# Kernel tuning notes

Hardware: AMD Instinct MI355X
Metric: run time of the kernel (lower is better)

The kernel has to match this reference:

```python
import jax, jax.numpy as jnp
import numpy as np

B, S, E, H, C = 16, 2048, 128, 768, 457


def setup_inputs() -> dict:
    key = jax.random.key(0)
    ks = jax.random.split(key, 8)
    hidden_states = jax.random.normal(ks[0], (B, S, H), dtype=jnp.float32)
    field_labels = jax.random.randint(ks[1], (B, S), 0, C, dtype=jnp.int64) if jax.config.jax_enable_x64 else jax.random.randint(ks[1], (B, S), 0, C, dtype=jnp.int32)
    label_masks = jax.random.randint(ks[2], (B, S), 0, 2, dtype=jnp.int32)
    entities_attr = jax.random.randint(ks[3], (B, E), 0, C, dtype=jnp.int32)
    entities_list = (jax.random.uniform(ks[4], (B, S, E)) < 0.05).astype(jnp.int32)
    entities_len = jnp.maximum(entities_list.sum(axis=1), 1).astype(jnp.int32)  # (B, E)
    entities_mask = jax.random.randint(ks[5], (B, E), 0, 2).astype(bool)
    W = jax.random.normal(ks[6], (C, H), dtype=jnp.float32) * 0.02
    b = jax.random.normal(ks[7], (C,), dtype=jnp.float32) * 0.02
    return {"hidden_states": hidden_states, "field_labels": field_labels,
            "label_masks": label_masks, "entities_attr": entities_attr,
            "entities_list": entities_list, "entities_len": entities_len,
            "entities_mask": entities_mask, "W": W, "b": b}


def reference(hidden_states, field_labels, label_masks, entities_attr,
              entities_list, entities_len, entities_mask, W, b):
    # Entity mean-pool: torch does (B,E,S,H) expand*mul->sum; algebraically a bmm.
    dt = hidden_states.dtype
    ent_hidden = jnp.einsum('bsh,bse->beh', hidden_states, entities_list.astype(dt))
    ent_hidden = ent_hidden / entities_len.astype(dt)[..., None]        # (B,E,H)
    mc_logits = jnp.einsum('beh,ch->bec', ent_hidden, W) + b             # (B,E,C)
    # masked CrossEntropyLoss (mean over selected entities)
    logp = jax.nn.log_softmax(mc_logits, axis=-1)
    nll = -jnp.take_along_axis(logp, entities_attr[..., None].astype(jnp.int32), axis=-1)[..., 0]
    m = entities_mask.astype(dt)
    mask_loss = (nll * m).sum() / m.sum()
    return mask_loss
```

## Files before the change

### kernel.cpp

```cpp
#include <hip/hip_runtime.h>
#include <hip/hip_bf16.h>
#include <cstdint>
#include <cstddef>

constexpr int Bn = 16, Sn = 2048, En = 128, Hn = 768, Cn = 457;
constexpr int NP = 512;
using f32x4  = __attribute__((ext_vector_type(4))) float;
using bf16x8 = __attribute__((ext_vector_type(8))) short;

static __device__ inline unsigned short f2bf(float x) {
  __hip_bfloat16 b = __float2bfloat16(x);
  return *reinterpret_cast<unsigned short*>(&b);
}
static __device__ inline float bflo(unsigned int u) {
  unsigned int v = u << 16;
  return *reinterpret_cast<float*>(&v);
}
static __device__ inline float bfhi(unsigned int u) {
  unsigned int v = u & 0xFFFF0000u;
  return *reinterpret_cast<float*>(&v);
}

#define LGKM_BAR()                                            \
  do {                                                        \
    asm volatile("s_waitcnt lgkmcnt(0)" ::: "memory");        \
    __builtin_amdgcn_sched_barrier(0);                        \
    __builtin_amdgcn_s_barrier();                             \
    __builtin_amdgcn_sched_barrier(0);                        \
  } while (0)

__global__ __launch_bounds__(256) void pack_k(
    const int* __restrict__ el, unsigned int* __restrict__ pk2)
{
  const int l = threadIdx.x & 63;
  const int gw = blockIdx.x * 4 + (threadIdx.x >> 6);
  #pragma unroll 8
  for (int j = 0; j < 8; ++j) {
    const int tok = gw * 8 + j;
    const int b = tok >> 11, s = tok & 2047;
    const int v0 = el[(size_t)tok * 128 + l];
    const int v1 = el[(size_t)tok * 128 + 64 + l];
    const unsigned long long b0 = __ballot(v0 != 0);
    const unsigned long long b1 = __ballot(v1 != 0);
    if (l == 0) {
      unsigned int* p = pk2 + (size_t)b * 4 * Sn + s;
      p[0]          = (unsigned int)b0;
      p[Sn]         = (unsigned int)(b0 >> 32);
      p[2 * Sn]     = (unsigned int)b1;
      p[3 * Sn]     = (unsigned int)(b1 >> 32);
    }
  }
}

constexpr int PBN = 32, PBK2 = 64, PLD2 = 72;
constexpr int SCH = 4, SLEN = Sn / SCH, PNK2 = SLEN / PBK2;
__global__ __launch_bounds__(256, 6) void pool_k(
    const float* __restrict__ hidden,
    const unsigned int* __restrict__ pk2,
    unsigned short* __restrict__ entp)
{
  const int b = blockIdx.x, n0 = blockIdx.y * PBN, sc = blockIdx.z;
  const int s0 = sc * SLEN;
  const int tid = threadIdx.x, l = tid & 63, wv = tid >> 6;
  const int wm = wv >> 1, wn = wv & 1;

  __shared__ unsigned short Bs[2][PBN][PLD2];
  __shared__ unsigned int   PK2[4 * SLEN];

  {
    const int w = tid >> 6, off = (tid & 63) * 8;
    const unsigned int* srcp =
        pk2 + (size_t)b * 4 * Sn + (size_t)w * Sn + s0 + off;
    *reinterpret_cast<uint4*>(&PK2[w * SLEN + off]) =
        *reinterpret_cast<const uint4*>(srcp);
    *reinterpret_cast<uint4*>(&PK2[w * SLEN + off + 4]) =
        *reinterpret_cast<const uint4*>(srcp + 4);
  }

  const float* hb = hidden + ((size_t)b * Sn + s0) * Hn + n0;
  const int g = wv * 2 + (l >> 5), col = l & 31;

  auto loadh = [&](int kk, float (&f)[8]) {
    const int sb = kk * PBK2 + g * 8;
    #pragma unroll
    for (int i = 0; i < 8; ++i)
      f[i] = hb[(size_t)(sb + i) * Hn + col];
  };

  auto stage_b = [&](int bsel, const float (&f)[8]) {
    uint2 d0, d1;
    d0.x = (unsigned int)f2bf(f[0]) | ((unsigned int)f2bf(f[1]) << 16);
    d0.y = (unsigned int)f2bf(f[2]) | ((unsigned int)f2bf(f[3]) << 16);
    d1.x = (unsigned int)f2bf(f[4]) | ((unsigned int)f2bf(f[5]) << 16);
    d1.y = (unsigned int)f2bf(f[6]) | ((unsigned int)f2bf(f[7]) << 16);
    *reinterpret_cast<uint2*>(&Bs[bsel][col][g * 8])     = d0;
    *reinterpret_cast<uint2*>(&Bs[bsel][col][g * 8 + 4]) = d1;
  };

  f32x4 acc[4] = {};
  const int rl = l & 15, q = l >> 4, kr = q * 8;

  auto mfma_step = [&](int k, int cur) {
    #pragma unroll
    for (int ks = 0; ks < 2; ++ks) {
      const int sbase = k * PBK2 + ks * 32 + kr;
      const bf16x8 bfr = *reinterpret_cast<const bf16x8*>(
          &Bs[cur][wn * 16 + rl][ks * 32 + kr]);
      #pragma unroll
      for (int mp = 0; mp < 2; ++mp) {
        const int w = wm * 2 + mp;
        const uint4 u0 = *reinterpret_cast<const uint4*>(&PK2[w * SLEN + sbase]);
        const uint4 u1 = *reinterpret_cast<const uint4*>(&PK2[w * SLEN + sbase + 4]);
        #pragma unroll
        for (int mh = 0; mh < 2; ++mh) {
          const int bi = mh * 16 + rl;
          bf16x8 afr;
          unsigned int* ap = reinterpret_cast<unsigned int*>(&afr);
          ap[0] = (((u0.x >> bi) & 1u) ? 0x3F80u : 0u) |
                  (((u0.y >> bi) & 1u) ? 0x3F800000u : 0u);
          ap[1] = (((u0.z >> bi) & 1u) ? 0x3F80u : 0u) |
                  (((u0.w >> bi) & 1u) ? 0x3F800000u : 0u);
          ap[2] = (((u1.x >> bi) & 1u) ? 0x3F80u : 0u) |
                  (((u1.y >> bi) & 1u) ? 0x3F800000u : 0u);
          ap[3] = (((u1.z >> bi) & 1u) ? 0x3F80u : 0u) |
                  (((u1.w >> bi) & 1u) ? 0x3F800000u : 0u);
          acc[mp * 2 + mh] = __builtin_amdgcn_mfma_f32_16x16x32_bf16(
              afr, bfr, acc[mp * 2 + mh], 0, 0, 0);
        }
      }
    }
  };

  float pf[3][8];
  loadh(0, pf[0]);
  loadh(1, pf[1]);
  LGKM_BAR();
  stage_b(0, pf[0]);
  LGKM_BAR();

  #pragma unroll
  for (int k = 0; k < PNK2; ++k) {
    if (k + 2 < PNK2) loadh(k + 2, pf[(k + 2) % 3]);
    mfma_step(k, k & 1);
    if (k + 1 < PNK2) {
      stage_b((k + 1) & 1, pf[(k + 1) % 3]);
      LGKM_BAR();
    }
  }

  unsigned short* dst = entp + (size_t)sc * Bn * En * Hn;
  const int rg = q * 4;
  const int colo = n0 + wn * 16 + rl;
  #pragma unroll
  for (int mi = 0; mi < 4; ++mi) {
    #pragma unroll
    for (int r = 0; r < 4; ++r) {
      const int e = wm * 64 + mi * 16 + rg + r;
      dst[(size_t)(b * En + e) * Hn + colo] = f2bf(acc[mi][r]);
    }
  }
}

__global__ __launch_bounds__(384) void fincast_k(
    const unsigned short* __restrict__ entp, const int* __restrict__ elen,
    const float* __restrict__ Wm,
    unsigned short* __restrict__ entbf, unsigned short* __restrict__ wbf)
{
  const int blk = blockIdx.x, t = threadIdx.x;
  if (blk < Bn * En) {
    const int be = blk;
    const float inv = 1.0f / (float)elen[be];
    constexpr size_t PSu = (size_t)Bn * En * Hn / 2;
    const unsigned int* src =
        reinterpret_cast<const unsigned int*>(entp) + (size_t)be * (Hn / 2) + t;
    float lo = 0.f, hi = 0.f;
    #pragma unroll
    for (int p = 0; p < SCH; ++p) {
      const unsigned int u = src[p * PSu];
      lo += bflo(u);
      hi += bfhi(u);
    }
    const unsigned int out = (unsigned int)f2bf(lo * inv) |
                             ((unsigned int)f2bf(hi * inv) << 16);
    reinterpret_cast<unsigned int*>(entbf)[(size_t)be * (Hn / 2) + t] = out;
  } else {
    const int c = blk - Bn * En;
    unsigned int out = 0u;
    if (c < Cn) {
      const float* wp = Wm + (size_t)c * Hn + 2 * t;
      out = (unsigned int)f2bf(wp[0]) | ((unsigned int)f2bf(wp[1]) << 16);
    }
    reinterpret_cast<unsigned int*>(wbf)[(size_t)c * (Hn / 2) + t] = out;
  }
}

constexpr int BM = 64, BN = 32, BK = 32, LDP = BK + 24;
__global__ __launch_bounds__(256) void gemm_k(
    const unsigned short* __restrict__ A,
    const unsigned short* __restrict__ Bm,
    float* __restrict__ Cm)
{
  __shared__ unsigned short As[BM][LDP];
  __shared__ unsigned short Bs[BN][LDP];
  const int bm = blockIdx.x, bn = blockIdx.y;
  const int tid = threadIdx.x, lane = tid & 63, wv = tid >> 6;
  const int wm = wv >> 1, wn = wv & 1;

  f32x4 acc[2] = {};

  for (int k0 = 0; k0 < Hn; k0 += BK) {
    {
      const int r = tid >> 2, kc = (tid & 3) * 8;
      const unsigned short* src = A + (size_t)(bm * BM + r) * Hn + k0 + kc;
      *reinterpret_cast<ulonglong2*>(&As[r][kc]) =
          *reinterpret_cast<const ulonglong2*>(src);
    }
    if (tid < 128) {
      const int r = tid >> 2, kc = (tid & 3) * 8;
      const unsigned short* src = Bm + (size_t)(bn * BN + r) * Hn + k0 + kc;
      *reinterpret_cast<ulonglong2*>(&Bs[r][kc]) =
          *reinterpret_cast<const ulonglong2*>(src);
    }
    __syncthreads();

    const int kr = (lane >> 4) * 8, rl = lane & 15;
    const bf16x8 bf = *reinterpret_cast<const bf16x8*>(&Bs[wn * 16 + rl][kr]);
    #pragma unroll
    for (int mi = 0; mi < 2; ++mi) {
      const bf16x8 af =
          *reinterpret_cast<const bf16x8*>(&As[wm * 32 + mi * 16 + rl][kr]);
      acc[mi] = __builtin_amdgcn_mfma_f32_16x16x32_bf16(af, bf, acc[mi], 0, 0, 0);
    }
    __syncthreads();
  }

  const int cl = lane & 15, rg = (lane >> 4) * 4;
  const int col = bn * BN + wn * 16 + cl;
  #pragma unroll
  for (int mi = 0; mi < 2; ++mi) {
    #pragma unroll
    for (int r = 0; r < 4; ++r) {
      const int row = bm * BM + wm * 32 + mi * 16 + rg + r;
      Cm[(size_t)row * NP + col] = acc[mi][r];
    }
  }
}

__global__ __launch_bounds__(256) void ce_k(
    const float* __restrict__ logits,
    const float* __restrict__ bv,
    const int* __restrict__ attr,
    const unsigned char* __restrict__ emask,
    float* __restrict__ nll)
{
  const int wv = threadIdx.x >> 6, lane = threadIdx.x & 63;
  const int be = blockIdx.x * 4 + wv;
  if (!emask[be]) { if (lane == 0) nll[be] = 0.f; return; }
  const float* row = logits + (size_t)be * NP;

  float mx = -3.4e38f;
  for (int i = lane; i < Cn; i += 64) mx = fmaxf(mx, row[i] + bv[i]);
  #pragma unroll
  for (int o = 32; o; o >>= 1) mx = fmaxf(mx, __shfl_xor(mx, o, 64));
  float sm = 0.f;
  for (int i = lane; i < Cn; i += 64) sm += __expf(row[i] + bv[i] - mx);
  #pragma unroll
  for (int o = 32; o; o >>= 1) sm += __shfl_xor(sm, o, 64);
  if (lane == 0) {
    const int tg = attr[be];
    nll[be] = mx + logf(sm) - (row[tg] + bv[tg]);
  }
}

__global__ __launch_bounds__(256) void reduce_k(
    const float* __restrict__ nll,
    const unsigned char* __restrict__ emask,
    float* __restrict__ out)
{
  const int tid = threadIdx.x;
  float s = 0.f, c = 0.f;
  for (int i = tid; i < Bn * En; i += 256) {
    s += nll[i];
    c += (float)emask[i];
  }
  #pragma unroll
  for (int o = 32; o; o >>= 1) {
    s += __shfl_xor(s, o, 64);
    c += __shfl_xor(c, o, 64);
  }
  __shared__ float ws_[4], wc_[4];
  const int wave = tid >> 6, lane = tid & 63;
  if (lane == 0) { ws_[wave] = s; wc_[wave] = c; }
  __syncthreads();
  if (tid == 0) {
    out[0] = (ws_[0] + ws_[1] + ws_[2] + ws_[3]) /
             (wc_[0] + wc_[1] + wc_[2] + wc_[3]);
  }
}

extern "C" void kernel_launch(void* const* d_in, const int* in_sizes, int n_in,
                              void* d_out, int out_size, void* d_ws, size_t ws_size,
                              hipStream_t stream) {
  const float* hidden        = (const float*)d_in[0];
  const int* attr            = (const int*)d_in[3];
  const int* el              = (const int*)d_in[4];
  const int* elen            = (const int*)d_in[5];
  const unsigned char* emask = (const unsigned char*)d_in[6];
  const float* Wm            = (const float*)d_in[7];
  const float* bv            = (const float*)d_in[8];

  unsigned short* entbf = (unsigned short*)d_ws;
  unsigned short* wbf   = entbf + (size_t)Bn * En * Hn;
  float* logits = (float*)(wbf + (size_t)NP * Hn);
  float* nll    = logits + (size_t)Bn * En * NP;
  unsigned int* pk2buf = (unsigned int*)(nll + Bn * En);
  unsigned short* entp =
      (unsigned short*)(pk2buf + (size_t)Bn * 4 * Sn);

  hipLaunchKernelGGL(pack_k, dim3(1024), dim3(256), 0, stream, el, pk2buf);
  hipLaunchKernelGGL(pool_k, dim3(Bn, Hn / PBN, SCH), dim3(256), 0, stream,
                     hidden, pk2buf, entp);
  hipLaunchKernelGGL(fincast_k, dim3(Bn * En + NP), dim3(384), 0, stream,
                     entp, elen, Wm, entbf, wbf);
  hipLaunchKernelGGL(gemm_k, dim3(Bn * En / BM, NP / BN), dim3(256), 0, stream,
                     entbf, wbf, logits);
  hipLaunchKernelGGL(ce_k, dim3(Bn * En / 4), dim3(256), 0, stream,
                     logits, bv, attr, emask, nll);
  hipLaunchKernelGGL(reduce_k, dim3(1), dim3(256), 0, stream,
                     nll, emask, (float*)d_out);
}
```

Baseline: 62.29 us.

## Fuse finalize, GEMM, cross-entropy and reduction into one cooperative kernel

Replaces four separate tail launches (finalize/cast, logits GEMM, per-row cross-entropy, final reduction) with a single cooperative kernel of 512 blocks that uses grid-wide syncs between phases. The goal is to remove per-kernel launch gaps and tail latency for these small kernels. In exchange it adds three grid barriers, shrinks the finalize phase to 256-thread blocks looping over tasks, and leaves only one block active for the final reduction.

```diff
diff --git a/kernel.cpp b/kernel.cpp
--- a/kernel.cpp
+++ b/kernel.cpp
@@ -1,7 +1,10 @@
 #include <hip/hip_runtime.h>
 #include <hip/hip_bf16.h>
+#include <hip/hip_cooperative_groups.h>
 #include <cstdint>
 #include <cstddef>
+
+namespace cg = cooperative_groups;
 
 constexpr int Bn = 16, Sn = 2048, En = 128, Hn = 768, Cn = 457;
 constexpr int NP = 512;
@@ -161,140 +164,148 @@
   }
 }
 
-__global__ __launch_bounds__(384) void fincast_k(
-    const unsigned short* __restrict__ entp, const int* __restrict__ elen,
+constexpr int BM = 64, BN = 32, BK = 32, LDP = BK + 24;
+__global__ __launch_bounds__(256) void tail_k(
+    const unsigned short* __restrict__ entp,
+    const int* __restrict__ elen,
     const float* __restrict__ Wm,
-    unsigned short* __restrict__ entbf, unsigned short* __restrict__ wbf)
-{
-  const int blk = blockIdx.x, t = threadIdx.x;
-  if (blk < Bn * En) {
-    const int be = blk;
-    const float inv = 1.0f / (float)elen[be];
-    constexpr size_t PSu = (size_t)Bn * En * Hn / 2;
-    const unsigned int* src =
-        reinterpret_cast<const unsigned int*>(entp) + (size_t)be * (Hn / 2) + t;
-    float lo = 0.f, hi = 0.f;
-    #pragma unroll
-    for (int p = 0; p < SCH; ++p) {
-      const unsigned int u = src[p * PSu];
-      lo += bflo(u);
-      hi += bfhi(u);
-    }
-    const unsigned int out = (unsigned int)f2bf(lo * inv) |
-                             ((unsigned int)f2bf(hi * inv) << 16);
-    reinterpret_cast<unsigned int*>(entbf)[(size_t)be * (Hn / 2) + t] = out;
-  } else {
-    const int c = blk - Bn * En;
-    unsigned int out = 0u;
-    if (c < Cn) {
-      const float* wp = Wm + (size_t)c * Hn + 2 * t;
-      out = (unsigned int)f2bf(wp[0]) | ((unsigned int)f2bf(wp[1]) << 16);
-    }
-    reinterpret_cast<unsigned int*>(wbf)[(size_t)c * (Hn / 2) + t] = out;
-  }
-}
-
-constexpr int BM = 64, BN = 32, BK = 32, LDP = BK + 24;
-__global__ __launch_bounds__(256) void gemm_k(
-    const unsigned short* __restrict__ A,
-    const unsigned short* __restrict__ Bm,
-    float* __restrict__ Cm)
-{
-  __shared__ unsigned short As[BM][LDP];
-  __shared__ unsigned short Bs[BN][LDP];
-  const int bm = blockIdx.x, bn = blockIdx.y;
-  const int tid = threadIdx.x, lane = tid & 63, wv = tid >> 6;
-  const int wm = wv >> 1, wn = wv & 1;
-
-  f32x4 acc[2] = {};
-
-  for (int k0 = 0; k0 < Hn; k0 += BK) {
-    {
-      const int r = tid >> 2, kc = (tid & 3) * 8;
-      const unsigned short* src = A + (size_t)(bm * BM + r) * Hn + k0 + kc;
-      *reinterpret_cast<ulonglong2*>(&As[r][kc]) =
-          *reinterpret_cast<const ulonglong2*>(src);
-    }
-    if (tid < 128) {
-      const int r = tid >> 2, kc = (tid & 3) * 8;
-      const unsigned short* src = Bm + (size_t)(bn * BN + r) * Hn + k0 + kc;
-      *reinterpret_cast<ulonglong2*>(&Bs[r][kc]) =
-          *reinterpret_cast<const ulonglong2*>(src);
-    }
-    __syncthreads();
-
-    const int kr = (lane >> 4) * 8, rl = lane & 15;
-    const bf16x8 bf = *reinterpret_cast<const bf16x8*>(&Bs[wn * 16 + rl][kr]);
-    #pragma unroll
-    for (int mi = 0; mi < 2; ++mi) {
-      const bf16x8 af =
-          *reinterpret_cast<const bf16x8*>(&As[wm * 32 + mi * 16 + rl][kr]);
-      acc[mi] = __builtin_amdgcn_mfma_f32_16x16x32_bf16(af, bf, acc[mi], 0, 0, 0);
-    }
-    __syncthreads();
-  }
-
-  const int cl = lane & 15, rg = (lane >> 4) * 4;
-  const int col = bn * BN + wn * 16 + cl;
-  #pragma unroll
-  for (int mi = 0; mi < 2; ++mi) {
-    #pragma unroll
-    for (int r = 0; r < 4; ++r) {
-      const int row = bm * BM + wm * 32 + mi * 16 + rg + r;
-      Cm[(size_t)row * NP + col] = acc[mi][r];
-    }
-  }
-}
-
-__global__ __launch_bounds__(256) void ce_k(
-    const float* __restrict__ logits,
     const float* __restrict__ bv,
     const int* __restrict__ attr,
     const unsigned char* __restrict__ emask,
-    float* __restrict__ nll)
-{
-  const int wv = threadIdx.x >> 6, lane = threadIdx.x & 63;
-  const int be = blockIdx.x * 4 + wv;
-  if (!emask[be]) { if (lane == 0) nll[be] = 0.f; return; }
-  const float* row = logits + (size_t)be * NP;
-
-  float mx = -3.4e38f;
-  for (int i = lane; i < Cn; i += 64) mx = fmaxf(mx, row[i] + bv[i]);
-  #pragma unroll
-  for (int o = 32; o; o >>= 1) mx = fmaxf(mx, __shfl_xor(mx, o, 64));
-  float sm = 0.f;
-  for (int i = lane; i < Cn; i += 64) sm += __expf(row[i] + bv[i] - mx);
-  #pragma unroll
-  for (int o = 32; o; o >>= 1) sm += __shfl_xor(sm, o, 64);
-  if (lane == 0) {
-    const int tg = attr[be];
-    nll[be] = mx + logf(sm) - (row[tg] + bv[tg]);
-  }
-}
-
-__global__ __launch_bounds__(256) void reduce_k(
-    const float* __restrict__ nll,
-    const unsigned char* __restrict__ emask,
+    unsigned short* __restrict__ entbf,
+    unsigned short* __restrict__ wbf,
+    float* __restrict__ logits,
+    float* __restrict__ nll,
     float* __restrict__ out)
 {
-  const int tid = threadIdx.x;
-  float s = 0.f, c = 0.f;
-  for (int i = tid; i < Bn * En; i += 256) {
-    s += nll[i];
-    c += (float)emask[i];
-  }
-  #pragma unroll
-  for (int o = 32; o; o >>= 1) {
-    s += __shfl_xor(s, o, 64);
-    c += __shfl_xor(c, o, 64);
-  }
+  cg::grid_group grid = cg::this_grid();
+  const int bid = blockIdx.x, tid = threadIdx.x;
+
+  __shared__ unsigned short As[BM][LDP];
+  __shared__ unsigned short Bs2[BN][LDP];
   __shared__ float ws_[4], wc_[4];
-  const int wave = tid >> 6, lane = tid & 63;
-  if (lane == 0) { ws_[wave] = s; wc_[wave] = c; }
-  __syncthreads();
-  if (tid == 0) {
-    out[0] = (ws_[0] + ws_[1] + ws_[2] + ws_[3]) /
-             (wc_[0] + wc_[1] + wc_[2] + wc_[3]);
+
+  for (int task = bid; task < Bn * En + NP; task += 512) {
+    if (task < Bn * En) {
+      const float inv = 1.0f / (float)elen[task];
+      constexpr size_t PSu = (size_t)Bn * En * Hn / 2;
+      const unsigned int* src =
+          reinterpret_cast<const unsigned int*>(entp) + (size_t)task * (Hn / 2);
+      unsigned int* dst =
+          reinterpret_cast<unsigned int*>(entbf) + (size_t)task * (Hn / 2);
+      for (int t = tid; t < Hn / 2; t += 256) {
+        float lo = 0.f, hi = 0.f;
+        #pragma unroll
+        for (int p = 0; p < SCH; ++p) {
+          const unsigned int u = src[t + p * PSu];
+          lo += bflo(u);
+          hi += bfhi(u);
+        }
+        dst[t] = (unsigned int)f2bf(lo * inv) |
+                 ((unsigned int)f2bf(hi * inv) << 16);
+      }
+    } else {
+      const int c = task - Bn * En;
+      unsigned int* dst =
+          reinterpret_cast<unsigned int*>(wbf) + (size_t)c * (Hn / 2);
+      for (int t = tid; t < Hn / 2; t += 256) {
+        unsigned int o = 0u;
+        if (c < Cn) {
+          const float* wp = Wm + (size_t)c * Hn + 2 * t;
+          o = (unsigned int)f2bf(wp[0]) | ((unsigned int)f2bf(wp[1]) << 16);
+        }
+        dst[t] = o;
+      }
+    }
+  }
+  grid.sync();
+
+  {
+    const int bm = bid >> 4, bn = bid & 15;
+    const int lane = tid & 63, wv = tid >> 6;
+    const int wm = wv >> 1, wn = wv & 1;
+    f32x4 acc[2] = {};
+
+    for (int k0 = 0; k0 < Hn; k0 += BK) {
+      {
+        const int r = tid >> 2, kc = (tid & 3) * 8;
+        const unsigned short* src = entbf + (size_t)(bm * BM + r) * Hn + k0 + kc;
+        *reinterpret_cast<ulonglong2*>(&As[r][kc]) =
+            *reinterpret_cast<const ulonglong2*>(src);
+      }
+      if (tid < 128) {
+        const int r = tid >> 2, kc = (tid & 3) * 8;
+        const unsigned short* src = wbf + (size_t)(bn * BN + r) * Hn + k0 + kc;
+        *reinterpret_cast<ulonglong2*>(&Bs2[r][kc]) =
+            *reinterpret_cast<const ulonglong2*>(src);
+      }
+      __syncthreads();
+
+      const int kr = (lane >> 4) * 8, rl = lane & 15;
+      const bf16x8 bf = *reinterpret_cast<const bf16x8*>(&Bs2[wn * 16 + rl][kr]);
+      #pragma unroll
+      for (int mi = 0; mi < 2; ++mi) {
+        const bf16x8 af =
+            *reinterpret_cast<const bf16x8*>(&As[wm * 32 + mi * 16 + rl][kr]);
+        acc[mi] = __builtin_amdgcn_mfma_f32_16x16x32_bf16(af, bf, acc[mi], 0, 0, 0);
+      }
+      __syncthreads();
+    }
+
+    const int cl = lane & 15, rg = (lane >> 4) * 4;
+    const int colo = bn * BN + wn * 16 + cl;
+    #pragma unroll
+    for (int mi = 0; mi < 2; ++mi) {
+      #pragma unroll
+      for (int r = 0; r < 4; ++r) {
+        const int row = bm * BM + wm * 32 + mi * 16 + rg + r;
+        logits[(size_t)row * NP + colo] = acc[mi][r];
+      }
+    }
+  }
+  grid.sync();
+
+  {
+    const int wv = tid >> 6, lane = tid & 63;
+    const int be = bid * 4 + wv;
+    if (emask[be]) {
+      const float* row = logits + (size_t)be * NP;
+      float mx = -3.4e38f;
+      for (int i = lane; i < Cn; i += 64) mx = fmaxf(mx, row[i] + bv[i]);
+      #pragma unroll
+      for (int o = 32; o; o >>= 1) mx = fmaxf(mx, __shfl_xor(mx, o, 64));
+      float sm = 0.f;
+      for (int i = lane; i < Cn; i += 64) sm += __expf(row[i] + bv[i] - mx);
+      #pragma unroll
+      for (int o = 32; o; o >>= 1) sm += __shfl_xor(sm, o, 64);
+      if (lane == 0) {
+        const int tg = attr[be];
+        nll[be] = mx + logf(sm) - (row[tg] + bv[tg]);
+      }
+    } else if (lane == 0) {
+      nll[be] = 0.f;
+    }
+  }
+  grid.sync();
+
+  if (bid == 0) {
+    float s = 0.f, c = 0.f;
+    for (int i = tid; i < Bn * En; i += 256) {
+      s += nll[i];
+      c += (float)emask[i];
+    }
+    #pragma unroll
+    for (int o = 32; o; o >>= 1) {
+      s += __shfl_xor(s, o, 64);
+      c += __shfl_xor(c, o, 64);
+    }
+    const int wave = tid >> 6, lane = tid & 63;
+    if (lane == 0) { ws_[wave] = s; wc_[wave] = c; }
+    __syncthreads();
+    if (tid == 0) {
+      out[0] = (ws_[0] + ws_[1] + ws_[2] + ws_[3]) /
+               (wc_[0] + wc_[1] + wc_[2] + wc_[3]);
+    }
   }
 }
 
@@ -316,16 +327,15 @@
   unsigned int* pk2buf = (unsigned int*)(nll + Bn * En);
   unsigned short* entp =
       (unsigned short*)(pk2buf + (size_t)Bn * 4 * Sn);
+  float* outp = (float*)d_out;
 
   hipLaunchKernelGGL(pack_k, dim3(1024), dim3(256), 0, stream, el, pk2buf);
   hipLaunchKernelGGL(pool_k, dim3(Bn, Hn / PBN, SCH), dim3(256), 0, stream,
                      hidden, pk2buf, entp);
-  hipLaunchKernelGGL(fincast_k, dim3(Bn * En + NP), dim3(384), 0, stream,
-                     entp, elen, Wm, entbf, wbf);
-  hipLaunchKernelGGL(gemm_k, dim3(Bn * En / BM, NP / BN), dim3(256), 0, stream,
-                     entbf, wbf, logits);
-  hipLaunchKernelGGL(ce_k, dim3(Bn * En / 4), dim3(256), 0, stream,
-                     logits, bv, attr, emask, nll);
-  hipLaunchKernelGGL(reduce_k, dim3(1), dim3(256), 0, stream,
-                     nll, emask, (float*)d_out);
-}
+
+  void* args[] = {(void*)&entp, (void*)&elen, (void*)&Wm, (void*)&bv,
+                  (void*)&attr, (void*)&emask, (void*)&entbf, (void*)&wbf,
+                  (void*)&logits, (void*)&nll, (void*)&outp};
+  hipLaunchCooperativeKernel((const void*)tail_k, dim3(512), dim3(256),
+                             args, 0, stream);
+}
```

Measured after the change: 224.6 us. +260.6%, slower.

## Fuse partial-sum finalize, logits GEMM and cross-entropy into one tail kernel

Applied to the files above, without the earlier changes.

The tail now runs as one kernel per 16-entity row block. It sums the split-S partials, scales by the inverse entity length into shared-memory bf16 A, computes all 512 logit columns with MFMA reading bf16 W straight from global memory, and does the softmax cross-entropy from shared memory. The W fp32-to-bf16 cast moves into pack_k. This removes two launches and the global logits and entbf round trips. The cost is only 128 blocks, each streaming the whole bf16 W from global/L2 without LDS tiling, and a large shared-memory footprint that may lower occupancy.

```diff
diff --git a/kernel.cpp b/kernel.cpp
--- a/kernel.cpp
+++ b/kernel.cpp
@@ -8,9 +8,9 @@
 using f32x4  = __attribute__((ext_vector_type(4))) float;
 using bf16x8 = __attribute__((ext_vector_type(8))) short;
 
-static __device__ inline unsigned short f2bf(float x) {
+static __device__ inline unsigned int f2bf(float x) {
   __hip_bfloat16 b = __float2bfloat16(x);
-  return *reinterpret_cast<unsigned short*>(&b);
+  return (unsigned int)*reinterpret_cast<unsigned short*>(&b);
 }
 static __device__ inline float bflo(unsigned int u) {
   unsigned int v = u << 16;
@@ -30,7 +30,8 @@
   } while (0)
 
 __global__ __launch_bounds__(256) void pack_k(
-    const int* __restrict__ el, unsigned int* __restrict__ pk2)
+    const int* __restrict__ el, const float* __restrict__ Wm,
+    unsigned int* __restrict__ pk2, unsigned short* __restrict__ wbf)
 {
   const int l = threadIdx.x & 63;
   const int gw = blockIdx.x * 4 + (threadIdx.x >> 6);
@@ -50,6 +51,18 @@
       p[3 * Sn]     = (unsigned int)(b1 >> 32);
     }
   }
+  const int c = blockIdx.x;
+  if (c < NP) {
+    unsigned int* dst = reinterpret_cast<unsigned int*>(wbf) + (size_t)c * (Hn / 2);
+    for (int t = threadIdx.x; t < Hn / 2; t += 256) {
+      unsigned int o = 0u;
+      if (c < Cn) {
+        const float* wp = Wm + (size_t)c * Hn + 2 * t;
+        o = f2bf(wp[0]) | (f2bf(wp[1]) << 16);
+      }
+      dst[t] = o;
+    }
+  }
 }
 
 constexpr int PBN = 32, PBK2 = 64, PLD2 = 72;
@@ -89,10 +102,10 @@
 
   auto stage_b = [&](int bsel, const float (&f)[8]) {
     uint2 d0, d1;
-    d0.x = (unsigned int)f2bf(f[0]) | ((unsigned int)f2bf(f[1]) << 16);
-    d0.y = (unsigned int)f2bf(f[2]) | ((unsigned int)f2bf(f[3]) << 16);
-    d1.x = (unsigned int)f2bf(f[4]) | ((unsigned int)f2bf(f[5]) << 16);
-    d1.y = (unsigned int)f2bf(f[6]) | ((unsigned int)f2bf(f[7]) << 16);
+    d0.x = f2bf(f[0]) | (f2bf(f[1]) << 16);
+    d0.y = f2bf(f[2]) | (f2bf(f[3]) << 16);
+    d1.x = f2bf(f[4]) | (f2bf(f[5]) << 16);
+    d1.y = f2bf(f[6]) | (f2bf(f[7]) << 16);
     *reinterpret_cast<uint2*>(&Bs[bsel][col][g * 8])     = d0;
     *reinterpret_cast<uint2*>(&Bs[bsel][col][g * 8 + 4]) = d1;
   };
@@ -156,119 +169,94 @@
     #pragma unroll
     for (int r = 0; r < 4; ++r) {
       const int e = wm * 64 + mi * 16 + rg + r;
-      dst[(size_t)(b * En + e) * Hn + colo] = f2bf(acc[mi][r]);
-    }
-  }
-}
-
-__global__ __launch_bounds__(384) void fincast_k(
-    const unsigned short* __restrict__ entp, const int* __restrict__ elen,
-    const float* __restrict__ Wm,
-    unsigned short* __restrict__ entbf, unsigned short* __restrict__ wbf)
-{
-  const int blk = blockIdx.x, t = threadIdx.x;
-  if (blk < Bn * En) {
-    const int be = blk;
-    const float inv = 1.0f / (float)elen[be];
-    constexpr size_t PSu = (size_t)Bn * En * Hn / 2;
-    const unsigned int* src =
-        reinterpret_cast<const unsigned int*>(entp) + (size_t)be * (Hn / 2) + t;
-    float lo = 0.f, hi = 0.f;
-    #pragma unroll
-    for (int p = 0; p < SCH; ++p) {
-      const unsigned int u = src[p * PSu];
-      lo += bflo(u);
-      hi += bfhi(u);
-    }
-    const unsigned int out = (unsigned int)f2bf(lo * inv) |
-                             ((unsigned int)f2bf(hi * inv) << 16);
-    reinterpret_cast<unsigned int*>(entbf)[(size_t)be * (Hn / 2) + t] = out;
-  } else {
-    const int c = blk - Bn * En;
-    unsigned int out = 0u;
-    if (c < Cn) {
-      const float* wp = Wm + (size_t)c * Hn + 2 * t;
-      out = (unsigned int)f2bf(wp[0]) | ((unsigned int)f2bf(wp[1]) << 16);
-    }
-    reinterpret_cast<unsigned int*>(wbf)[(size_t)c * (Hn / 2) + t] = out;
-  }
-}
-
-constexpr int BM = 64, BN = 32, BK = 32, LDP = BK + 24;
-__global__ __launch_bounds__(256) void gemm_k(
-    const unsigned short* __restrict__ A,
-    const unsigned short* __restrict__ Bm,
-    float* __restrict__ Cm)
-{
-  __shared__ unsigned short As[BM][LDP];
-  __shared__ unsigned short Bs[BN][LDP];
-  const int bm = blockIdx.x, bn = blockIdx.y;
-  const int tid = threadIdx.x, lane = tid & 63, wv = tid >> 6;
-  const int wm = wv >> 1, wn = wv & 1;
-
-  f32x4 acc[2] = {};
-
-  for (int k0 = 0; k0 < Hn; k0 += BK) {
-    {
-      const int r = tid >> 2, kc = (tid & 3) * 8;
-      const unsigned short* src = A + (size_t)(bm * BM + r) * Hn + k0 + kc;
-      *reinterpret_cast<ulonglong2*>(&As[r][kc]) =
-          *reinterpret_cast<const ulonglong2*>(src);
-    }
-    if (tid < 128) {
-      const int r = tid >> 2, kc = (tid & 3) * 8;
-      const unsigned short* src = Bm + (size_t)(bn * BN + r) * Hn + k0 + kc;
-      *reinterpret_cast<ulonglong2*>(&Bs[r][kc]) =
-          *reinterpret_cast<const ulonglong2*>(src);
-    }
-    __syncthreads();
-
-    const int kr = (lane >> 4) * 8, rl = lane & 15;
-    const bf16x8 bf = *reinterpret_cast<const bf16x8*>(&Bs[wn * 16 + rl][kr]);
-    #pragma unroll
-    for (int mi = 0; mi < 2; ++mi) {
-      const bf16x8 af =
-          *reinterpret_cast<const bf16x8*>(&As[wm * 32 + mi * 16 + rl][kr]);
-      acc[mi] = __builtin_amdgcn_mfma_f32_16x16x32_bf16(af, bf, acc[mi], 0, 0, 0);
-    }
-    __syncthreads();
-  }
-
-  const int cl = lane & 15, rg = (lane >> 4) * 4;
-  const int col = bn * BN + wn * 16 + cl;
-  #pragma unroll
-  for (int mi = 0; mi < 2; ++mi) {
-    #pragma unroll
-    for (int r = 0; r < 4; ++r) {
-      const int row = bm * BM + wm * 32 + mi * 16 + rg + r;
-      Cm[(size_t)row * NP + col] = acc[mi][r];
-    }
-  }
-}
-
-__global__ __launch_bounds__(256) void ce_k(
-    const float* __restrict__ logits,
+      dst[(size_t)(b * En + e) * Hn + colo] = (unsigned short)f2bf(acc[mi][r]);
+    }
+  }
+}
+
+__global__ __launch_bounds__(256) void tail16_k(
+    const unsigned short* __restrict__ entp,
+    const int* __restrict__ elen,
+    const unsigned short* __restrict__ wbf,
     const float* __restrict__ bv,
     const int* __restrict__ attr,
     const unsigned char* __restrict__ emask,
     float* __restrict__ nll)
 {
-  const int wv = threadIdx.x >> 6, lane = threadIdx.x & 63;
-  const int be = blockIdx.x * 4 + wv;
-  if (!emask[be]) { if (lane == 0) nll[be] = 0.f; return; }
-  const float* row = logits + (size_t)be * NP;
-
-  float mx = -3.4e38f;
-  for (int i = lane; i < Cn; i += 64) mx = fmaxf(mx, row[i] + bv[i]);
+  const int bm = blockIdx.x;
+  const int tid = threadIdx.x, lane = tid & 63, wv = tid >> 6;
+
+  __shared__ unsigned short A[16][776];
+  __shared__ float lg[16][520];
+  __shared__ float invl[16];
+
+  if (tid < 16) invl[tid] = 1.0f / (float)elen[bm * 16 + tid];
+  __syncthreads();
+
+  {
+    constexpr size_t PSu = (size_t)Bn * En * Hn / 2;
+    const unsigned int* src =
+        reinterpret_cast<const unsigned int*>(entp) + (size_t)bm * 16 * (Hn / 2);
+    for (int idx = tid; idx < 16 * (Hn / 2); idx += 256) {
+      const int row = idx / (Hn / 2), u = idx - row * (Hn / 2);
+      float lo = 0.f, hi = 0.f;
+      #pragma unroll
+      for (int p = 0; p < SCH; ++p) {
+        const unsigned int v = src[idx + p * PSu];
+        lo += bflo(v);
+        hi += bfhi(v);
+      }
+      const float iv = invl[row];
+      *reinterpret_cast<unsigned int*>(&A[row][2 * u]) =
+          f2bf(lo * iv) | (f2bf(hi * iv) << 16);
+    }
+  }
+  __syncthreads();
+
+  const int rl = lane & 15, q = lane >> 4, kr = q * 8;
+  const int colBase = wv * 128;
+  f32x4 acc[8] = {};
+  for (int k0 = 0; k0 < Hn; k0 += 32) {
+    const bf16x8 af = *reinterpret_cast<const bf16x8*>(&A[rl][k0 + kr]);
+    #pragma unroll
+    for (int ni = 0; ni < 8; ++ni) {
+      const int c = colBase + ni * 16 + rl;
+      const bf16x8 bfr = *reinterpret_cast<const bf16x8*>(
+          wbf + (size_t)c * Hn + k0 + kr);
+      acc[ni] = __builtin_amdgcn_mfma_f32_16x16x32_bf16(af, bfr, acc[ni], 0, 0, 0);
+    }
+  }
+
+  {
+    const int rg = q * 4;
+    #pragma unroll
+    for (int ni = 0; ni < 8; ++ni)
+      #pragma unroll
+      for (int r = 0; r < 4; ++r)
+        lg[rg + r][colBase + ni * 16 + rl] = acc[ni][r];
+  }
+  __syncthreads();
+
   #pragma unroll
-  for (int o = 32; o; o >>= 1) mx = fmaxf(mx, __shfl_xor(mx, o, 64));
-  float sm = 0.f;
-  for (int i = lane; i < Cn; i += 64) sm += __expf(row[i] + bv[i] - mx);
-  #pragma unroll
-  for (int o = 32; o; o >>= 1) sm += __shfl_xor(sm, o, 64);
-  if (lane == 0) {
-    const int tg = attr[be];
-    nll[be] = mx + logf(sm) - (row[tg] + bv[tg]);
+  for (int j = 0; j < 4; ++j) {
+    const int r = wv * 4 + j;
+    const int be = bm * 16 + r;
+    if (emask[be]) {
+      float mx = -3.4e38f;
+      for (int i = lane; i < Cn; i += 64) mx = fmaxf(mx, lg[r][i] + bv[i]);
+      #pragma unroll
+      for (int o = 32; o; o >>= 1) mx = fmaxf(mx, __shfl_xor(mx, o, 64));
+      float sm = 0.f;
+      for (int i = lane; i < Cn; i += 64) sm += __expf(lg[r][i] + bv[i] - mx);
+      #pragma unroll
+      for (int o = 32; o; o >>= 1) sm += __shfl_xor(sm, o, 64);
+      if (lane == 0) {
+        const int tg = attr[be];
+        nll[be] = mx + logf(sm) - (lg[r][tg] + bv[tg]);
+      }
+    } else if (lane == 0) {
+      nll[be] = 0.f;
+    }
   }
 }
 
@@ -309,23 +297,18 @@
   const float* Wm            = (const float*)d_in[7];
   const float* bv            = (const float*)d_in[8];
 
-  unsigned short* entbf = (unsigned short*)d_ws;
-  unsigned short* wbf   = entbf + (size_t)Bn * En * Hn;
-  float* logits = (float*)(wbf + (size_t)NP * Hn);
-  float* nll    = logits + (size_t)Bn * En * NP;
+  unsigned short* wbf = (unsigned short*)d_ws;
+  float* nll = (float*)(wbf + (size_t)NP * Hn);
   unsigned int* pk2buf = (unsigned int*)(nll + Bn * En);
   unsigned short* entp =
       (unsigned short*)(pk2buf + (size_t)Bn * 4 * Sn);
 
-  hipLaunchKernelGGL(pack_k, dim3(1024), dim3(256), 0, stream, el, pk2buf);
+  hipLaunchKernelGGL(pack_k, dim3(1024), dim3(256), 0, stream,
+                     el, Wm, pk2buf, wbf);
   hipLaunchKernelGGL(pool_k, dim3(Bn, Hn / PBN, SCH), dim3(256), 0, stream,
                      hidden, pk2buf, entp);
-  hipLaunchKernelGGL(fincast_k, dim3(Bn * En + NP), dim3(384), 0, stream,
-                     entp, elen, Wm, entbf, wbf);
-  hipLaunchKernelGGL(gemm_k, dim3(Bn * En / BM, NP / BN), dim3(256), 0, stream,
-                     entbf, wbf, logits);
-  hipLaunchKernelGGL(ce_k, dim3(Bn * En / 4), dim3(256), 0, stream,
-                     logits, bv, attr, emask, nll);
+  hipLaunchKernelGGL(tail16_k, dim3(Bn * En / 16), dim3(256), 0, stream,
+                     entp, elen, wbf, bv, attr, emask, nll);
   hipLaunchKernelGGL(reduce_k, dim3(1), dim3(256), 0, stream,
                      nll, emask, (float*)d_out);
 }
```

Measured after the change: 69.77 us. 12.0% more time.
